# Kernel tuning notes

Measured on AMD Instinct MI355X. Metric: run time of the kernel, lower is better.

Reference implementation:

```python
import jax, jax.numpy as jnp
import numpy as np

DIM = 512
HEADS = 8
HEAD_DIM = DIM // HEADS
R = 2  # reduce_ratio
SCALE = HEAD_DIM ** -0.5


def setup_inputs() -> dict:
    key = jax.random.key(0)
    ks = jax.random.split(key, 8)
    bs, H, W = 4, 64, 64
    n = H * W
    std = 0.02
    x = jax.random.normal(ks[0], (bs, n, DIM), dtype=jnp.float32)
    q_w = jax.random.normal(ks[1], (DIM, DIM), dtype=jnp.float32) * std
    kv_w = jax.random.normal(ks[2], (DIM, 2 * DIM), dtype=jnp.float32) * std
    proj_w = jax.random.normal(ks[3], (DIM, DIM), dtype=jnp.float32) * std
    proj_b = jnp.zeros((DIM,), dtype=jnp.float32)
    # Conv2d(dim, dim, kernel=R, stride=R), kaiming-like init
    fan_out = R * R * DIM
    sr_w = jax.random.normal(ks[4], (DIM, DIM, R, R), dtype=jnp.float32) * np.sqrt(2.0 / fan_out)
    sr_b = jnp.zeros((DIM,), dtype=jnp.float32)
    ln_w = jnp.ones((DIM,), dtype=jnp.float32)
    ln_b = jnp.zeros((DIM,), dtype=jnp.float32)
    return {"x": x, "q_w": q_w, "kv_w": kv_w, "proj_w": proj_w, "proj_b": proj_b,
            "sr_w": sr_w, "sr_b": sr_b, "ln_w": ln_w, "ln_b": ln_b, "H": H, "W": W}


def _layernorm(x, w, b, eps=1e-5):
    mu = jnp.mean(x, axis=-1, keepdims=True)
    var = jnp.var(x, axis=-1, keepdims=True)
    return (x - mu) * jax.lax.rsqrt(var + eps) * w + b


def reference(x, q_w, kv_w, proj_w, proj_b, sr_w, sr_b, ln_w, ln_b, H, W):
    bs, n, ch = x.shape
    # q: (bs, heads, n, head_dim)
    q = (x @ q_w).reshape(bs, n, HEADS, HEAD_DIM).transpose(0, 2, 1, 3)
    # spatial reduction of kv source: strided conv + layernorm
    x_img = x.transpose(0, 2, 1).reshape(bs, ch, H, W)
    xr = jax.lax.conv_general_dilated(
        x_img, sr_w, window_strides=(R, R), padding='VALID',
        dimension_numbers=('NCHW', 'OIHW', 'NCHW')) + sr_b[None, :, None, None]
    xr = xr.reshape(bs, ch, -1).transpose(0, 2, 1)  # (bs, n_kv, ch)
    xr = _layernorm(xr, ln_w, ln_b)
    kv = xr @ kv_w  # (bs, n_kv, 2*ch)
    n_kv = kv.shape[1]
    kv = kv.reshape(bs, n_kv, 2, HEADS, HEAD_DIM).transpose(2, 0, 3, 1, 4)
    k, v = kv[0], kv[1]  # (bs, heads, n_kv, head_dim)
    att = jnp.einsum('bhqd,bhkd->bhqk', q, k) * SCALE
    att = jax.nn.softmax(att, axis=-1)
    net = jnp.einsum('bhqk,bhkd->bhqd', att, v)
    net = net.transpose(0, 2, 1, 3).reshape(bs, n, ch)
    return net @ proj_w + proj_b
```

## Files before the change

### kernel.cpp

```cpp
#include <hip/hip_runtime.h>
#include <cstdint>

#define HEADS 8
#define HD 64
#define NQ 4096
#define NKV 1024

typedef unsigned short u16;
typedef __attribute__((ext_vector_type(8))) short short8;
typedef __attribute__((ext_vector_type(4))) float f32x4;
typedef __attribute__((ext_vector_type(16))) float f32x16;

__device__ __forceinline__ u16 f2bf(float f){
  union { float f; unsigned u; } c; c.f = f;
  unsigned r = c.u + 0x7fffu + ((c.u >> 16) & 1u);
  return (u16)(r >> 16);
}
__device__ __forceinline__ unsigned pack2(float a, float b){
  return (unsigned)f2bf(a) | ((unsigned)f2bf(b) << 16);
}
__device__ __forceinline__ float fexp2(float x){
  float r;
  asm("v_exp_f32 %0, %1" : "=v"(r) : "v"(x));
  return r;
}
__device__ __forceinline__ unsigned cvtpk(float a, float b){
  unsigned r;
  asm("v_cvt_pk_bf16_f32 %0, %1, %2" : "=v"(r) : "v"(a), "v"(b));
  return r;
}
__device__ __forceinline__ void gll16(const void* g, void* l){
  __builtin_amdgcn_global_load_lds((const __attribute__((address_space(1))) unsigned*)g,
                                   (__attribute__((address_space(3))) unsigned*)l, 16, 0, 0);
}
#define SB0() __builtin_amdgcn_sched_barrier(0)
#define MFMA16(a, b, c) __builtin_amdgcn_mfma_f32_16x16x32_bf16(a, b, c, 0, 0, 0)
#define MFMA32(a, b, c) __builtin_amdgcn_mfma_f32_32x32x16_bf16(a, b, c, 0, 0, 0)
#define Z16 {0.f,0.f,0.f,0.f,0.f,0.f,0.f,0.f,0.f,0.f,0.f,0.f,0.f,0.f,0.f,0.f}

__global__ __launch_bounds__(256) void prep_all(const float* __restrict__ x,
                                                const float* __restrict__ q_w,
                                                const float* __restrict__ kv_w,
                                                const float* __restrict__ proj_w,
                                                const float* __restrict__ sr_w,
                                                u16* __restrict__ x_bf,
                                                u16* __restrict__ q_wT, u16* __restrict__ kv_wT,
                                                u16* __restrict__ proj_wT, u16* __restrict__ conv_BT){
  int bid = blockIdx.x;
  if (bid < 4096){
    int tid = bid * 256 + threadIdx.x;
    size_t src = (size_t)tid * 8;
    const float4* s4 = (const float4*)(x + src);
    float4 v0 = s4[0], v1 = s4[1];
    uint4 p;
    p.x = pack2(v0.x, v0.y); p.y = pack2(v0.z, v0.w);
    p.z = pack2(v1.x, v1.y); p.w = pack2(v1.z, v1.w);
    *(uint4*)(x_bf + src) = p;
    return;
  }
  int e = (bid - 4096) * 256 + threadIdx.x;
  if (e < 262144){ int n = e >> 9, k = e & 511; q_wT[e] = f2bf(q_w[k * 512 + n]); return; }
  e -= 262144;
  if (e < 524288){ int n = e >> 9, k = e & 511; kv_wT[e] = f2bf(kv_w[k * 1024 + n]); return; }
  e -= 524288;
  if (e < 262144){ int n = e >> 9, k = e & 511; proj_wT[e] = f2bf(proj_w[k * 512 + n]); return; }
  e -= 262144;
  { int co = e >> 11, r = e & 2047, t = r >> 9, ci = r & 511;
    conv_BT[e] = f2bf(sr_w[co * 2048 + ci * 4 + t]); }
}

__global__ __launch_bounds__(256) void gemm_qconv(const u16* __restrict__ x_bf, const u16* __restrict__ q_wT,
                                                  const u16* __restrict__ conv_BT,
                                                  u16* __restrict__ q_sb, float* __restrict__ xr_pre,
                                                  const float* __restrict__ sr_b){
  __shared__ __align__(16) u16 As[128 * 64];
  __shared__ __align__(16) u16 Bs[128 * 64];
  const int tid = threadIdx.x, lane = tid & 63, wave = tid >> 6;
  const int l15 = lane & 15, g = lane >> 4, r7 = l15 & 7;
  const int wr = wave >> 1, wc = wave & 1;
  int y = blockIdx.y;
  const bool isQ = (y < 128);
  int kz = 0, m0, kb = 0, iters, KB;
  const u16* BT;
  if (isQ){ m0 = y * 128; iters = 8;  KB = 512;  BT = q_wT; }
  else { y -= 128; kz = y >> 5; m0 = (y & 31) * 128; kb = kz << 10; iters = 16; KB = 2048; BT = conv_BT; }
  const int n0 = blockIdx.x * 128;

  unsigned aBase[4], bBase[4];
  #pragma unroll
  for (int ii = 0; ii < 4; ++ii){
    int c = ii * 256 + tid;
    int row = c >> 3, sc = (c & 7) ^ (row & 7);
    if (isQ) aBase[ii] = (unsigned)(m0 + row) * 512 + sc * 8;
    else { int grow = m0 + row, b = grow >> 10, pr = grow & 1023;
           aBase[ii] = ((unsigned)(b * 4096) + (pr >> 5) * 128 + (pr & 31) * 2) * 512 + sc * 8; }
    bBase[ii] = (unsigned)(n0 + row) * KB + sc * 8;
  }

  f32x4 acc[4][4] = {};
  for (int i = 0; i < iters; ++i){
    int kt = kb + i * 64;
    unsigned aOff;
    if (isQ) aOff = kt;
    else { int t = kt >> 9; aOff = (unsigned)((t >> 1) * 64 + (t & 1)) * 512 + (kt & 511); }
    #pragma unroll
    for (int ii = 0; ii < 4; ++ii){
      gll16(x_bf + aBase[ii] + aOff, As + (size_t)(ii * 256 + wave * 64) * 8);
      gll16(BT + bBase[ii] + kt,     Bs + (size_t)(ii * 256 + wave * 64) * 8);
    }
    __syncthreads();
    #pragma unroll
    for (int kk = 0; kk < 2; ++kk){
      short8 af[4];
      #pragma unroll
      for (int mi = 0; mi < 4; ++mi)
        af[mi] = *(const short8*)(As + (wr * 64 + mi * 16 + l15) * 64 + (((kk * 4 + g) ^ r7) << 3));
      #pragma unroll
      for (int ni = 0; ni < 4; ++ni){
        short8 bf = *(const short8*)(Bs + (wc * 64 + ni * 16 + l15) * 64 + (((kk * 4 + g) ^ r7) << 3));
        #pragma unroll
        for (int mi = 0; mi < 4; ++mi)
          acc[mi][ni] = MFMA16(af[mi], bf, acc[mi][ni]);
      }
    }
    __syncthreads();
  }
  #pragma unroll
  for (int mi = 0; mi < 4; ++mi){
    int row = m0 + wr * 64 + mi * 16 + (lane >> 4) * 4;
    #pragma unroll
    for (int ni = 0; ni < 4; ++ni){
      int col = n0 + wc * 64 + ni * 16 + l15;
      f32x4 v = acc[mi][ni];
      if (isQ){
        int h = col >> 6, d = col & 63;
        #pragma unroll
        for (int j = 0; j < 4; ++j){
          int r = row + j, b = r >> 12, nq = r & 4095;
          q_sb[(((size_t)(b * HEADS + h)) * NQ + nq) * HD + d] = f2bf(v[j] * 0.18033688f);
        }
      } else {
        float* Co = xr_pre + (size_t)kz * 4096 * 512;
        float bb = (kz == 0) ? sr_b[col] : 0.f;
        #pragma unroll
        for (int j = 0; j < 4; ++j) Co[(size_t)(row + j) * 512 + col] = v[j] + bb;
      }
    }
  }
}

template<int MODE>
__global__ __launch_bounds__(256) void gemm_bt(const u16* __restrict__ A, const u16* __restrict__ BT,
                                               float* __restrict__ Cf,
                                               u16* __restrict__ Cb0,
                                               u16* __restrict__ Cb1, const float* __restrict__ bias,
                                               int M, int N, int K){
  __shared__ __align__(16) u16 As[128 * 64];
  __shared__ __align__(16) u16 Bs[128 * 64];
  const int tid = threadIdx.x, lane = tid & 63, wave = tid >> 6;
  const int l15 = lane & 15, g = lane >> 4, r7 = l15 & 7;
  const int m0 = blockIdx.y * 128, n0 = blockIdx.x * 128;
  const int wr = wave >> 1, wc = wave & 1;
  f32x4 acc[4][4] = {};
  for (int kt = 0; kt < K; kt += 64){
    #pragma unroll
    for (int i = 0; i < 4; ++i){
      int c = i * 256 + tid;
      int row = c >> 3, sc = (c & 7) ^ (row & 7);
      gll16(A  + (size_t)(m0 + row) * K + kt + sc * 8, As + (size_t)(i * 256 + wave * 64) * 8);
      gll16(BT + (size_t)(n0 + row) * K + kt + sc * 8, Bs + (size_t)(i * 256 + wave * 64) * 8);
    }
    __syncthreads();
    #pragma unroll
    for (int kk = 0; kk < 2; ++kk){
      short8 af[4];
      #pragma unroll
      for (int mi = 0; mi < 4; ++mi)
        af[mi] = *(const short8*)(As + (wr * 64 + mi * 16 + l15) * 64 + (((kk * 4 + g) ^ r7) << 3));
      #pragma unroll
      for (int ni = 0; ni < 4; ++ni){
        short8 bf = *(const short8*)(Bs + (wc * 64 + ni * 16 + l15) * 64 + (((kk * 4 + g) ^ r7) << 3));
        #pragma unroll
        for (int mi = 0; mi < 4; ++mi)
          acc[mi][ni] = MFMA16(af[mi], bf, acc[mi][ni]);
      }
    }
    __syncthreads();
  }
  #pragma unroll
  for (int mi = 0; mi < 4; ++mi){
    int row = m0 + wr * 64 + mi * 16 + (lane >> 4) * 4;
    #pragma unroll
    for (int ni = 0; ni < 4; ++ni){
      int col = n0 + wc * 64 + ni * 16 + l15;
      f32x4 v = acc[mi][ni];
      if (MODE == 0){
        float bb = bias ? bias[col] : 0.f;
        #pragma unroll
        for (int j = 0; j < 4; ++j) Cf[(size_t)(row + j) * N + col] = v[j] + bb;
      } else {
        int s = col >> 9, h = (col >> 6) & 7, d = col & 63;
        if (s == 0){
          #pragma unroll
          for (int j = 0; j < 4; ++j){
            int r = row + j, b = r >> 10, p = r & 1023;
            Cb0[(((size_t)(b * HEADS + h)) * NKV + p) * HD + d] = f2bf(v[j]);
          }
        } else {
          int b = row >> 10, p0 = row & 1023;
          int pp = (p0 & ~12) | (((p0 >> 2) & 1) << 3) | (((p0 >> 3) & 1) << 2);
          ushort4 pk;
          pk.x = f2bf(v[0]); pk.y = f2bf(v[1]); pk.z = f2bf(v[2]); pk.w = f2bf(v[3]);
          *(ushort4*)(Cb1 + (((size_t)(b * HEADS + h)) * HD + d) * NKV + pp) = pk;
        }
      }
    }
  }
}

__global__ __launch_bounds__(256) void ln_k(const float* __restrict__ xp,
                                            const float* __restrict__ w,
                                            const float* __restrict__ bias, u16* __restrict__ xr){
  int row = blockIdx.x * 4 + (threadIdx.x >> 6);
  int lane = threadIdx.x & 63;
  const float* s1 = xp + (size_t)row * 512;
  const float* s2 = s1 + (size_t)4096 * 512;
  float vals[8]; float s = 0.f, ss = 0.f;
  #pragma unroll
  for (int j = 0; j < 8; ++j){
    int c = lane + j * 64;
    float v = s1[c] + s2[c];
    vals[j] = v; s += v; ss += v * v;
  }
  #pragma unroll
  for (int off = 32; off >= 1; off >>= 1){ s += __shfl_xor(s, off); ss += __shfl_xor(ss, off); }
  float mean = s * (1.f / 512.f);
  float var  = ss * (1.f / 512.f) - mean * mean;
  float rs = rsqrtf(var + 1e-5f);
  u16* dst = xr + (size_t)row * 512;
  #pragma unroll
  for (int j = 0; j < 8; ++j){
    int c = lane + j * 64;
    dst[c] = f2bf((vals[j] - mean) * rs * w[c] + bias[c]);
  }
}

template<bool LAST>
__device__ __forceinline__ void attn_tile(const u16* ksb, const u16* vsb,
                                          u16* kstage, u16* vstage,
                                          const u16* akg, const u16* avg,
                                          const short8* qf,
                                          int l31, int hi, int x7,
                                          f32x16* o, float& l_run){
  asm volatile("s_waitcnt vmcnt(0)" ::: "memory");
  __builtin_amdgcn_s_barrier();
  SB0();

  if (!LAST){
    gll16(akg,              kstage);
    gll16(akg + 2048,       kstage + 2048);
    gll16(avg,              vstage);
    gll16(avg + 32 * 1024,  vstage + 2048);
  }
  SB0();

  f32x16 sa[2];
  __builtin_amdgcn_s_setprio(1);
  #pragma unroll
  for (int sub = 0; sub < 2; ++sub){
    f32x16 a = Z16;
    #pragma unroll
    for (int ks = 0; ks < 4; ++ks){
      short8 kf = *(const short8*)(ksb + (sub * 32 + l31) * 64 + (((ks * 2 + hi) ^ x7) << 3));
      a = MFMA32(kf, qf[ks], a);
    }
    sa[sub] = a;
  }
  __builtin_amdgcn_s_setprio(0);

  unsigned w[16];
  float ps = 0.f;
  #pragma unroll
  for (int sub = 0; sub < 2; ++sub)
    #pragma unroll
    for (int t = 0; t < 8; ++t){
      float p0 = fexp2(sa[sub][2 * t]), p1 = fexp2(sa[sub][2 * t + 1]);
      ps += p0 + p1;
      w[sub * 8 + t] = cvtpk(p0, p1);
    }
  l_run += ps;

  __builtin_amdgcn_s_setprio(1);
  #pragma unroll
  for (int dt = 0; dt < 2; ++dt)
    #pragma unroll
    for (int sl = 0; sl < 4; ++sl){
      short8 vf = *(const short8*)(vsb + (dt * 32 + l31) * 64 + (((sl * 2 + hi) ^ x7) << 3));
      union { unsigned u[4]; short8 s; } bb;
      bb.u[0] = w[sl * 4 + 0]; bb.u[1] = w[sl * 4 + 1];
      bb.u[2] = w[sl * 4 + 2]; bb.u[3] = w[sl * 4 + 3];
      o[dt] = MFMA32(vf, bb.s, o[dt]);
    }
  __builtin_amdgcn_s_setprio(0);
  SB0();
}

__global__ __launch_bounds__(256) void attn_k(const u16* __restrict__ q_s, const u16* __restrict__ k_s,
                                              const u16* __restrict__ vt_s, u16* __restrict__ net){
  __shared__ __align__(16) u16 Ks[2][64 * 64];
  __shared__ __align__(16) u16 Vt[2][64 * 64];
  const int tid = threadIdx.x, lane = tid & 63, wave = tid >> 6;
  const int l31 = lane & 31, hi = lane >> 5, x7 = lane & 7;
  const int id = blockIdx.x;
  const int xcd = id & 7, slot = id >> 3;
  const int bh = 4 * xcd + (slot >> 5);
  const int qblk = slot & 31;
  const u16* kb  = k_s  + (size_t)bh * NKV * HD;
  const u16* vtb = vt_s + (size_t)bh * HD * NKV;
  const int q0 = qblk * 128 + wave * 32;
  const u16* qbase = q_s + ((size_t)bh * NQ + q0 + l31) * HD + hi * 8;
  short8 qf[4];
  #pragma unroll
  for (int ks = 0; ks < 4; ++ks) qf[ks] = *(const short8*)(qbase + ks * 16);

  const int swz8 = (((tid & 7) ^ ((tid >> 3) & 7)) << 3);
  const u16* ak0 = kb  + (size_t)(tid >> 3) * 64   + swz8;
  const u16* av0 = vtb + (size_t)(tid >> 3) * 1024 + swz8;

  f32x16 o[2] = { Z16, Z16 };
  float l_run = 0.f;

  gll16(ak0,             &Ks[0][wave * 512]);
  gll16(ak0 + 2048,      &Ks[0][2048 + wave * 512]);
  gll16(av0,             &Vt[0][wave * 512]);
  gll16(av0 + 32 * 1024, &Vt[0][2048 + wave * 512]);

  for (int tt = 0; tt < 7; ++tt){
    attn_tile<false>(&Ks[0][0], &Vt[0][0], &Ks[1][wave * 512], &Vt[1][wave * 512],
                     ak0 + (size_t)(2 * tt + 1) * 4096, av0 + (2 * tt + 1) * 64,
                     qf, l31, hi, x7, o, l_run);
    attn_tile<false>(&Ks[1][0], &Vt[1][0], &Ks[0][wave * 512], &Vt[0][wave * 512],
                     ak0 + (size_t)(2 * tt + 2) * 4096, av0 + (2 * tt + 2) * 64,
                     qf, l31, hi, x7, o, l_run);
  }
  attn_tile<false>(&Ks[0][0], &Vt[0][0], &Ks[1][wave * 512], &Vt[1][wave * 512],
                   ak0 + (size_t)15 * 4096, av0 + 15 * 64,
                   qf, l31, hi, x7, o, l_run);
  attn_tile<true>(&Ks[1][0], &Vt[1][0], nullptr, nullptr, nullptr, nullptr,
                  qf, l31, hi, x7, o, l_run);

  float l = l_run + __shfl_xor(l_run, 32);
  float inv = 1.f / l;
  int b = bh >> 3, h = bh & 7;
  size_t obase = ((size_t)b * NQ + q0 + l31) * 512 + h * 64;
  #pragma unroll
  for (int dt = 0; dt < 2; ++dt)
    #pragma unroll
    for (int t = 0; t < 8; ++t){
      int j = 2 * t;
      int d = dt * 32 + (j & 3) + 8 * (j >> 2) + 4 * hi;
      *(unsigned*)(net + obase + d) = cvtpk(o[dt][j] * inv, o[dt][j + 1] * inv);
    }
}

extern "C" void kernel_launch(void* const* d_in, const int* in_sizes, int n_in,
                              void* d_out, int out_size, void* d_ws, size_t ws_size,
                              hipStream_t stream){
  const float* x      = (const float*)d_in[0];
  const float* q_w    = (const float*)d_in[1];
  const float* kv_w   = (const float*)d_in[2];
  const float* proj_w = (const float*)d_in[3];
  const float* proj_b = (const float*)d_in[4];
  const float* sr_w   = (const float*)d_in[5];
  const float* sr_b   = (const float*)d_in[6];
  const float* ln_w   = (const float*)d_in[7];
  const float* ln_b   = (const float*)d_in[8];
  (void)in_sizes; (void)n_in; (void)out_size; (void)ws_size;

  char* ws = (char*)d_ws;
  u16*   x_bf    = (u16*)(ws);
  u16*   xr      = (u16*)(ws + ((size_t)16 << 20));
  u16*   net     = (u16*)(ws + ((size_t)16 << 20));
  u16*   q_sb    = (u16*)(ws + ((size_t)32 << 20));
  float* xr_pre  = (float*)(ws + ((size_t)48 << 20));
  u16*   k_sb    = (u16*)(ws + ((size_t)48 << 20));
  u16*   vt_sb   = (u16*)(ws + ((size_t)52 << 20));
  u16*   q_wT    = (u16*)(ws + ((size_t)64 << 20));
  u16*   kv_wT   = (u16*)(ws + ((size_t)64 << 20) + 524288);
  u16*   proj_wT = (u16*)(ws + ((size_t)64 << 20) + 524288 + 1048576);
  u16*   conv_BT = (u16*)(ws + ((size_t)64 << 20) + 524288 + 1048576 + 524288);
  float* out = (float*)d_out;

  prep_all<<<12288, 256, 0, stream>>>(x, q_w, kv_w, proj_w, sr_w,
                                      x_bf, q_wT, kv_wT, proj_wT, conv_BT);
  gemm_qconv<<<dim3(4, 192), 256, 0, stream>>>(x_bf, q_wT, conv_BT, q_sb, xr_pre, sr_b);
  ln_k<<<1024, 256, 0, stream>>>(xr_pre, ln_w, ln_b, xr);
  gemm_bt<2><<<dim3(8, 32),  256, 0, stream>>>(xr, kv_wT, nullptr, k_sb, vt_sb, nullptr, 4096, 1024, 512);
  attn_k<<<1024, 256, 0, stream>>>(q_sb, k_sb, vt_sb, net);
  gemm_bt<0><<<dim3(4, 128), 256, 0, stream>>>(net, proj_wT, out, nullptr, nullptr, proj_b, 16384, 512, 512);
}
```

Measured before the change: 140.4 us.

## Compute softmax row sums via MFMA, reorder QK before prefetch, split KV GEMM tiles

The attention tile now runs the QK^T MFMAs before issuing the next tile's global-to-LDS prefetch. The per-lane exp-sum plus final cross-lane shuffle is replaced by an extra MFMA against a ones vector that accumulates row sums in the matrix unit. The KV projection GEMM gets its own kernel with 64-row M tiles, doubling the grid from 256 to 512 blocks for better CU occupancy, and the output projection GEMM is split out as a plain kernel. The ones-MFMA adds matrix work and a 16-register accumulator per tile, which may raise register pressure.

After: 133.8 us. 4.7% less time.

```diff
diff --git a/kernel.cpp b/kernel.cpp
--- a/kernel.cpp
+++ b/kernel.cpp
@@ -149,12 +149,73 @@
   }
 }
 
-template<int MODE>
-__global__ __launch_bounds__(256) void gemm_bt(const u16* __restrict__ A, const u16* __restrict__ BT,
-                                               float* __restrict__ Cf,
-                                               u16* __restrict__ Cb0,
-                                               u16* __restrict__ Cb1, const float* __restrict__ bias,
-                                               int M, int N, int K){
+__global__ __launch_bounds__(256) void gemm_kv(const u16* __restrict__ A, const u16* __restrict__ BT,
+                                               u16* __restrict__ Cb0, u16* __restrict__ Cb1){
+  __shared__ __align__(16) u16 As[64 * 64];
+  __shared__ __align__(16) u16 Bs[128 * 64];
+  const int tid = threadIdx.x, lane = tid & 63, wave = tid >> 6;
+  const int l15 = lane & 15, g = lane >> 4, r7 = l15 & 7;
+  const int m0 = blockIdx.y * 64, n0 = blockIdx.x * 128;
+  const int wr = wave >> 1, wc = wave & 1;
+  f32x4 acc[2][4] = {};
+  for (int kt = 0; kt < 512; kt += 64){
+    #pragma unroll
+    for (int i = 0; i < 2; ++i){
+      int c = i * 256 + tid;
+      int row = c >> 3, sc = (c & 7) ^ (row & 7);
+      gll16(A + (size_t)(m0 + row) * 512 + kt + sc * 8, As + (size_t)(i * 256 + wave * 64) * 8);
+    }
+    #pragma unroll
+    for (int i = 0; i < 4; ++i){
+      int c = i * 256 + tid;
+      int row = c >> 3, sc = (c & 7) ^ (row & 7);
+      gll16(BT + (size_t)(n0 + row) * 512 + kt + sc * 8, Bs + (size_t)(i * 256 + wave * 64) * 8);
+    }
+    __syncthreads();
+    #pragma unroll
+    for (int kk = 0; kk < 2; ++kk){
+      short8 af[2];
+      #pragma unroll
+      for (int mi = 0; mi < 2; ++mi)
+        af[mi] = *(const short8*)(As + (wr * 32 + mi * 16 + l15) * 64 + (((kk * 4 + g) ^ r7) << 3));
+      #pragma unroll
+      for (int ni = 0; ni < 4; ++ni){
+        short8 bf = *(const short8*)(Bs + (wc * 64 + ni * 16 + l15) * 64 + (((kk * 4 + g) ^ r7) << 3));
+        #pragma unroll
+        for (int mi = 0; mi < 2; ++mi)
+          acc[mi][ni] = MFMA16(af[mi], bf, acc[mi][ni]);
+      }
+    }
+    __syncthreads();
+  }
+  #pragma unroll
+  for (int mi = 0; mi < 2; ++mi){
+    int row = m0 + wr * 32 + mi * 16 + (lane >> 4) * 4;
+    #pragma unroll
+    for (int ni = 0; ni < 4; ++ni){
+      int col = n0 + wc * 64 + ni * 16 + l15;
+      f32x4 v = acc[mi][ni];
+      int s = col >> 9, h = (col >> 6) & 7, d = col & 63;
+      if (s == 0){
+        #pragma unroll
+        for (int j = 0; j < 4; ++j){
+          int r = row + j, b = r >> 10, p = r & 1023;
+          Cb0[(((size_t)(b * HEADS + h)) * NKV + p) * HD + d] = f2bf(v[j]);
+        }
+      } else {
+        int b = row >> 10, p0 = row & 1023;
+        int pp = (p0 & ~12) | (((p0 >> 2) & 1) << 3) | (((p0 >> 3) & 1) << 2);
+        ushort4 pk;
+        pk.x = f2bf(v[0]); pk.y = f2bf(v[1]); pk.z = f2bf(v[2]); pk.w = f2bf(v[3]);
+        *(ushort4*)(Cb1 + (((size_t)(b * HEADS + h)) * HD + d) * NKV + pp) = pk;
+      }
+    }
+  }
+}
+
+__global__ __launch_bounds__(256) void gemm_proj(const u16* __restrict__ A, const u16* __restrict__ BT,
+                                                 float* __restrict__ Cf, const float* __restrict__ bias,
+                                                 int M, int N, int K){
   __shared__ __align__(16) u16 As[128 * 64];
   __shared__ __align__(16) u16 Bs[128 * 64];
   const int tid = threadIdx.x, lane = tid & 63, wave = tid >> 6;
@@ -194,26 +255,9 @@
     for (int ni = 0; ni < 4; ++ni){
       int col = n0 + wc * 64 + ni * 16 + l15;
       f32x4 v = acc[mi][ni];
-      if (MODE == 0){
-        float bb = bias ? bias[col] : 0.f;
-        #pragma unroll
-        for (int j = 0; j < 4; ++j) Cf[(size_t)(row + j) * N + col] = v[j] + bb;
-      } else {
-        int s = col >> 9, h = (col >> 6) & 7, d = col & 63;
-        if (s == 0){
-          #pragma unroll
-          for (int j = 0; j < 4; ++j){
-            int r = row + j, b = r >> 10, p = r & 1023;
-            Cb0[(((size_t)(b * HEADS + h)) * NKV + p) * HD + d] = f2bf(v[j]);
-          }
-        } else {
-          int b = row >> 10, p0 = row & 1023;
-          int pp = (p0 & ~12) | (((p0 >> 2) & 1) << 3) | (((p0 >> 3) & 1) << 2);
-          ushort4 pk;
-          pk.x = f2bf(v[0]); pk.y = f2bf(v[1]); pk.z = f2bf(v[2]); pk.w = f2bf(v[3]);
-          *(ushort4*)(Cb1 + (((size_t)(b * HEADS + h)) * HD + d) * NKV + pp) = pk;
-        }
-      }
+      float bb = bias[col];
+      #pragma unroll
+      for (int j = 0; j < 4; ++j) Cf[(size_t)(row + j) * N + col] = v[j] + bb;
     }
   }
 }
@@ -249,11 +293,26 @@
 __device__ __forceinline__ void attn_tile(const u16* ksb, const u16* vsb,
                                           u16* kstage, u16* vstage,
                                           const u16* akg, const u16* avg,
-                                          const short8* qf,
+                                          const short8* qf, short8 ones,
                                           int l31, int hi, int x7,
-                                          f32x16* o, float& l_run){
+                                          f32x16* o, f32x16& ol){
   asm volatile("s_waitcnt vmcnt(0)" ::: "memory");
   __builtin_amdgcn_s_barrier();
+  SB0();
+
+  f32x16 sa[2];
+  __builtin_amdgcn_s_setprio(1);
+  #pragma unroll
+  for (int sub = 0; sub < 2; ++sub){
+    f32x16 a = Z16;
+    #pragma unroll
+    for (int ks = 0; ks < 4; ++ks){
+      short8 kf = *(const short8*)(ksb + (sub * 32 + l31) * 64 + (((ks * 2 + hi) ^ x7) << 3));
+      a = MFMA32(kf, qf[ks], a);
+    }
+    sa[sub] = a;
+  }
+  __builtin_amdgcn_s_setprio(0);
   SB0();
 
   if (!LAST){
@@ -264,43 +323,26 @@
   }
   SB0();
 
-  f32x16 sa[2];
+  unsigned w[16];
+  #pragma unroll
+  for (int sub = 0; sub < 2; ++sub)
+    #pragma unroll
+    for (int t = 0; t < 8; ++t)
+      w[sub * 8 + t] = cvtpk(fexp2(sa[sub][2 * t]), fexp2(sa[sub][2 * t + 1]));
+
   __builtin_amdgcn_s_setprio(1);
   #pragma unroll
-  for (int sub = 0; sub < 2; ++sub){
-    f32x16 a = Z16;
-    #pragma unroll
-    for (int ks = 0; ks < 4; ++ks){
-      short8 kf = *(const short8*)(ksb + (sub * 32 + l31) * 64 + (((ks * 2 + hi) ^ x7) << 3));
-      a = MFMA32(kf, qf[ks], a);
-    }
-    sa[sub] = a;
-  }
-  __builtin_amdgcn_s_setprio(0);
-
-  unsigned w[16];
-  float ps = 0.f;
-  #pragma unroll
-  for (int sub = 0; sub < 2; ++sub)
-    #pragma unroll
-    for (int t = 0; t < 8; ++t){
-      float p0 = fexp2(sa[sub][2 * t]), p1 = fexp2(sa[sub][2 * t + 1]);
-      ps += p0 + p1;
-      w[sub * 8 + t] = cvtpk(p0, p1);
-    }
-  l_run += ps;
-
-  __builtin_amdgcn_s_setprio(1);
-  #pragma unroll
-  for (int dt = 0; dt < 2; ++dt)
-    #pragma unroll
-    for (int sl = 0; sl < 4; ++sl){
+  for (int sl = 0; sl < 4; ++sl){
+    union { unsigned u[4]; short8 s; } bb;
+    bb.u[0] = w[sl * 4 + 0]; bb.u[1] = w[sl * 4 + 1];
+    bb.u[2] = w[sl * 4 + 2]; bb.u[3] = w[sl * 4 + 3];
+    #pragma unroll
+    for (int dt = 0; dt < 2; ++dt){
       short8 vf = *(const short8*)(vsb + (dt * 32 + l31) * 64 + (((sl * 2 + hi) ^ x7) << 3));
-      union { unsigned u[4]; short8 s; } bb;
-      bb.u[0] = w[sl * 4 + 0]; bb.u[1] = w[sl * 4 + 1];
-      bb.u[2] = w[sl * 4 + 2]; bb.u[3] = w[sl * 4 + 3];
       o[dt] = MFMA32(vf, bb.s, o[dt]);
     }
+    ol = MFMA32(ones, bb.s, ol);
+  }
   __builtin_amdgcn_s_setprio(0);
   SB0();
 }
@@ -322,13 +364,14 @@
   short8 qf[4];
   #pragma unroll
   for (int ks = 0; ks < 4; ++ks) qf[ks] = *(const short8*)(qbase + ks * 16);
+  const short8 ones = {0x3F80, 0x3F80, 0x3F80, 0x3F80, 0x3F80, 0x3F80, 0x3F80, 0x3F80};
 
   const int swz8 = (((tid & 7) ^ ((tid >> 3) & 7)) << 3);
   const u16* ak0 = kb  + (size_t)(tid >> 3) * 64   + swz8;
   const u16* av0 = vtb + (size_t)(tid >> 3) * 1024 + swz8;
 
   f32x16 o[2] = { Z16, Z16 };
-  float l_run = 0.f;
+  f32x16 ol = Z16;
 
   gll16(ak0,             &Ks[0][wave * 512]);
   gll16(ak0 + 2048,      &Ks[0][2048 + wave * 512]);
@@ -338,19 +381,18 @@
   for (int tt = 0; tt < 7; ++tt){
     attn_tile<false>(&Ks[0][0], &Vt[0][0], &Ks[1][wave * 512], &Vt[1][wave * 512],
                      ak0 + (size_t)(2 * tt + 1) * 4096, av0 + (2 * tt + 1) * 64,
-                     qf, l31, hi, x7, o, l_run);
+                     qf, ones, l31, hi, x7, o, ol);
     attn_tile<false>(&Ks[1][0], &Vt[1][0], &Ks[0][wave * 512], &Vt[0][wave * 512],
                      ak0 + (size_t)(2 * tt + 2) * 4096, av0 + (2 * tt + 2) * 64,
-                     qf, l31, hi, x7, o, l_run);
+                     qf, ones, l31, hi, x7, o, ol);
   }
   attn_tile<false>(&Ks[0][0], &Vt[0][0], &Ks[1][wave * 512], &Vt[1][wave * 512],
                    ak0 + (size_t)15 * 4096, av0 + 15 * 64,
-                   qf, l31, hi, x7, o, l_run);
+                   qf, ones, l31, hi, x7, o, ol);
   attn_tile<true>(&Ks[1][0], &Vt[1][0], nullptr, nullptr, nullptr, nullptr,
-                  qf, l31, hi, x7, o, l_run);
-
-  float l = l_run + __shfl_xor(l_run, 32);
-  float inv = 1.f / l;
+                  qf, ones, l31, hi, x7, o, ol);
+
+  float inv = 1.f / ol[0];
   int b = bh >> 3, h = bh & 7;
   size_t obase = ((size_t)b * NQ + q0 + l31) * 512 + h * 64;
   #pragma unroll
@@ -395,7 +437,7 @@
                                       x_bf, q_wT, kv_wT, proj_wT, conv_BT);
   gemm_qconv<<<dim3(4, 192), 256, 0, stream>>>(x_bf, q_wT, conv_BT, q_sb, xr_pre, sr_b);
   ln_k<<<1024, 256, 0, stream>>>(xr_pre, ln_w, ln_b, xr);
-  gemm_bt<2><<<dim3(8, 32),  256, 0, stream>>>(xr, kv_wT, nullptr, k_sb, vt_sb, nullptr, 4096, 1024, 512);
+  gemm_kv<<<dim3(8, 64), 256, 0, stream>>>(xr, kv_wT, k_sb, vt_sb);
   attn_k<<<1024, 256, 0, stream>>>(q_sb, k_sb, vt_sb, net);
-  gemm_bt<0><<<dim3(4, 128), 256, 0, stream>>>(net, proj_wT, out, nullptr, nullptr, proj_b, 16384, 512, 512);
-}
+  gemm_proj<<<dim3(4, 128), 256, 0, stream>>>(net, proj_wT, out, proj_b, 16384, 512, 512);
+}
```
